# Kernel optimization log

Measured on AMD Instinct MI355X. Metric: run time of the kernel, lower is better.

## Reference

```python
import jax, jax.numpy as jnp
import numpy as np

T, B, D, O = 2048, 32, 512, 512


def setup_inputs() -> dict:
    key = jax.random.key(0)
    ks = jax.random.split(key, 12)
    s = 0.02
    return {
        "word": jax.random.normal(ks[0], (T, B, D), dtype=jnp.float32),
        "Wf": jax.random.normal(ks[1], (D, D), dtype=jnp.float32) * s,
        "bf": jax.random.normal(ks[2], (D,), dtype=jnp.float32) * s,
        "Wi": jax.random.normal(ks[3], (D, D), dtype=jnp.float32) * s,
        "bi": jax.random.normal(ks[4], (D,), dtype=jnp.float32) * s,
        "Wz": jax.random.normal(ks[5], (D, D), dtype=jnp.float32) * s,
        "bz": jax.random.normal(ks[6], (D,), dtype=jnp.float32) * s,
        "Wo": jax.random.normal(ks[7], (D, D), dtype=jnp.float32) * s,
        "bo": jax.random.normal(ks[8], (D,), dtype=jnp.float32) * s,
        "Wy": jax.random.normal(ks[9], (O, D), dtype=jnp.float32) * s,
        "by": jax.random.normal(ks[10], (O,), dtype=jnp.float32) * s,
    }


def reference(word, Wf, bf, Wi, bi, Wz, bz, Wo, bo, Wy, by):
    # Faithful to the original buggy module:
    #  - forward discards the updated cell state, so c == 0 every step and
    #    the zf gate (wf) never affects the output.
    #  - z and zo reuse wi(hidden) instead of wz/wo(hidden).
    #  - the same Linear is applied to letter and hidden, so bias is doubled
    #    in zi (and zf).
    Bsz, Dd = word.shape[1], word.shape[2]

    def step(h, x):  # h: [B, D], x: [B, D]
        hWi = h @ Wi.T                                  # reused by zi, z, zo
        zi = jax.nn.sigmoid(x @ Wi.T + hWi + 2.0 * bi)
        z = jax.nn.sigmoid(x @ Wz.T + bz + hWi + bi)
        zo = jax.nn.sigmoid(x @ Wo.T + bo + hWi + bi)
        c = zi * z                                      # zf * 0 + zi * z
        h_new = zo * jnp.tanh(c)
        return h_new, None

    h0 = jnp.zeros((Bsz, Dd), dtype=word.dtype)
    h_final, _ = jax.lax.scan(step, h0, word)
    # original computes wy(hidden) every step but only returns the last one
    output = h_final @ Wy.T + by                        # [B, O]
    return output
```

## Files before the change

kernel.cpp:

```cpp
#include <hip/hip_runtime.h>

typedef unsigned int u32;
typedef unsigned short u16;
typedef _Float16 f16;
typedef f16 f16x2 __attribute__((ext_vector_type(2)));

__device__ __forceinline__ float fdot2(u32 a, u32 b, float c) {
#if __has_builtin(__builtin_amdgcn_fdot2)
    return __builtin_amdgcn_fdot2(__builtin_bit_cast(f16x2, a),
                                  __builtin_bit_cast(f16x2, b), c, false);
#else
    f16x2 av = __builtin_bit_cast(f16x2, a), bv = __builtin_bit_cast(f16x2, b);
    c += (float)av[0] * (float)bv[0];
    c += (float)av[1] * (float)bv[1];
    return c;
#endif
}

__device__ __forceinline__ u32 pack2h(float a, float b) {
    f16x2 h; h[0] = (f16)a; h[1] = (f16)b;
    return __builtin_bit_cast(u32, h);
}
__device__ __forceinline__ float h2f(u16 x) { return (float)__builtin_bit_cast(f16, x); }
__device__ __forceinline__ u16 f2h(float x) { f16 h = (f16)x; return __builtin_bit_cast(u16, h); }

__device__ __forceinline__ float fexp(float x) {
#if __has_builtin(__builtin_amdgcn_exp2f)
    return __builtin_amdgcn_exp2f(x * 1.44269504088896f);
#else
    return __expf(x);
#endif
}
__device__ __forceinline__ float frcp(float x) {
#if __has_builtin(__builtin_amdgcn_rcpf)
    return __builtin_amdgcn_rcpf(x);
#else
    return 1.0f / x;
#endif
}
__device__ __forceinline__ float fsigmoid(float x) { return frcp(1.0f + fexp(-x)); }
__device__ __forceinline__ float ftanh_pos(float x) { return 1.0f - 2.0f * frcp(fexp(2.0f * x) + 1.0f); }

__global__ __launch_bounds__(512) void k0_pack(const float* __restrict__ Wi,
                                               const float* __restrict__ Wy,
                                               u32* __restrict__ Wpk,
                                               u32* __restrict__ Wypk) {
    const int p = blockIdx.x & 255;
    const int d = threadIdx.x;
    const float* src = (blockIdx.x < 256) ? Wi : Wy;
    u32* dst = (blockIdx.x < 256) ? Wpk : Wypk;
    float v0 = src[(size_t)d * 512 + 2 * p];
    float v1 = src[(size_t)d * 512 + 2 * p + 1];
    dst[(size_t)p * 512 + d] = pack2h(v0, v1);
}

__global__ __launch_bounds__(256) void k1_gates(
    const float* __restrict__ word,
    const float* __restrict__ Wi, const float* __restrict__ Wz, const float* __restrict__ Wo,
    const float* __restrict__ bi, const float* __restrict__ bz, const float* __restrict__ bo,
    u16* __restrict__ Xi, u16* __restrict__ Xz, u16* __restrict__ Xo)
{
    __shared__ u32 ws2[3][32][132];
    __shared__ u32 xs2[2][32][36];

    const int tid = threadIdx.x;
    const int d_l = tid & 63;
    const int bq  = tid >> 6;
    const int t0  = blockIdx.x * 2;
    const int d0  = blockIdx.y * 128;

    const float* Wg[3] = {Wi, Wz, Wo};

    float acc[2][2][8][3];
    #pragma unroll
    for (int tt = 0; tt < 2; ++tt)
        #pragma unroll
        for (int db = 0; db < 2; ++db)
            #pragma unroll
            for (int j = 0; j < 8; ++j)
                #pragma unroll
                for (int g = 0; g < 3; ++g) acc[tt][db][j][g] = 0.0f;

    for (int k0 = 0; k0 < 512; k0 += 64) {
        {
            const int p = tid & 31, bg = tid >> 5;
            #pragma unroll
            for (int tt = 0; tt < 2; ++tt)
                #pragma unroll
                for (int j = 0; j < 4; ++j) {
                    int b = bg * 4 + j;
                    const float2 v = *(const float2*)(word + (((size_t)(t0 + tt) * 32 + b) * 512 + k0 + 2 * p));
                    xs2[tt][p][b] = pack2h(v.x, v.y);
                }
        }
        {
            const int q = tid & 15, r = tid >> 4;
            #pragma unroll
            for (int g = 0; g < 3; ++g)
                #pragma unroll
                for (int s = 0; s < 8; ++s) {
                    int i = r + 16 * s;
                    const float4 v = *(const float4*)(Wg[g] + ((size_t)(d0 + i) * 512 + k0 + 4 * q));
                    ws2[g][2 * q + 0][i] = pack2h(v.x, v.y);
                    ws2[g][2 * q + 1][i] = pack2h(v.z, v.w);
                }
        }
        __syncthreads();
        #pragma unroll 2
        for (int p = 0; p < 32; ++p) {
            u32 x2[2][8];
            #pragma unroll
            for (int tt = 0; tt < 2; ++tt) {
                const uint4* xr = (const uint4*)&xs2[tt][p][bq * 8];
                uint4 xa = xr[0], xb = xr[1];
                x2[tt][0] = xa.x; x2[tt][1] = xa.y; x2[tt][2] = xa.z; x2[tt][3] = xa.w;
                x2[tt][4] = xb.x; x2[tt][5] = xb.y; x2[tt][6] = xb.z; x2[tt][7] = xb.w;
            }
            u32 w2[3][2];
            #pragma unroll
            for (int g = 0; g < 3; ++g) {
                w2[g][0] = ws2[g][p][d_l];
                w2[g][1] = ws2[g][p][d_l + 64];
            }
            #pragma unroll
            for (int tt = 0; tt < 2; ++tt)
                #pragma unroll
                for (int db = 0; db < 2; ++db)
                    #pragma unroll
                    for (int j = 0; j < 8; ++j)
                        #pragma unroll
                        for (int g = 0; g < 3; ++g)
                            acc[tt][db][j][g] = fdot2(x2[tt][j], w2[g][db], acc[tt][db][j][g]);
        }
        __syncthreads();
    }

    #pragma unroll
    for (int db = 0; db < 2; ++db) {
        const int d = d0 + 64 * db + d_l;
        const float b0 = 2.0f * bi[d];
        const float b1 = bz[d] + bi[d];
        const float b2 = bo[d] + bi[d];
        #pragma unroll
        for (int tt = 0; tt < 2; ++tt)
            #pragma unroll
            for (int j = 0; j < 8; ++j) {
                const size_t o = ((size_t)(t0 + tt) * 32 + (bq * 8 + j)) * 512 + d;
                Xi[o] = f2h(acc[tt][db][j][0] + b0);
                Xz[o] = f2h(acc[tt][db][j][1] + b1);
                Xo[o] = f2h(acc[tt][db][j][2] + b2);
            }
    }
}

__global__ __launch_bounds__(512, 2) void k2_recur(
    const u16* __restrict__ Xi, const u16* __restrict__ Xz, const u16* __restrict__ Xo,
    const u32* __restrict__ Wpk, const u32* __restrict__ Wypk,
    const float* __restrict__ by, float* __restrict__ out)
{
    __shared__ u32 wlds[28][512];
    __shared__ alignas(16) u16 hbuf[2][512];

    const int b = blockIdx.x;
    const int tid = threadIdx.x;

    u32 w[228];
    #pragma unroll
    for (int p = 0; p < 228; ++p) w[p] = Wpk[(size_t)p * 512 + tid];
    #pragma unroll
    for (int j = 0; j < 28; ++j) wlds[j][tid] = Wpk[(size_t)(228 + j) * 512 + tid];

    hbuf[0][tid] = (u16)0;
    __syncthreads();

    size_t idx0 = ((size_t)0 * 32 + b) * 512 + tid;
    u16 xi_c = Xi[idx0], xz_c = Xz[idx0], xo_c = Xo[idx0];

    for (int t = 0; t < 2048; ++t) {
        const int cur = t & 1, nxt = cur ^ 1;
        const int tn = (t + 1) & 2047;
        const size_t idxn = ((size_t)tn * 32 + b) * 512 + tid;
        u16 xi_n = Xi[idxn], xz_n = Xz[idxn], xo_n = Xo[idxn];

        const uint4* hv = (const uint4*)&hbuf[cur][0];
        float a0 = 0.f, a1 = 0.f, a2 = 0.f, a3 = 0.f;
        #pragma unroll
        for (int j = 0; j < 57; ++j) {
            uint4 hc = hv[j];
            a0 = fdot2(hc.x, w[4 * j + 0], a0);
            a1 = fdot2(hc.y, w[4 * j + 1], a1);
            a2 = fdot2(hc.z, w[4 * j + 2], a2);
            a3 = fdot2(hc.w, w[4 * j + 3], a3);
        }
        #pragma unroll
        for (int j = 57; j < 64; ++j) {
            uint4 hc = hv[j];
            const int q = 4 * (j - 57);
            a0 = fdot2(hc.x, wlds[q + 0][tid], a0);
            a1 = fdot2(hc.y, wlds[q + 1][tid], a1);
            a2 = fdot2(hc.z, wlds[q + 2][tid], a2);
            a3 = fdot2(hc.w, wlds[q + 3][tid], a3);
        }
        const float v = (a0 + a1) + (a2 + a3);

        const float zi = fsigmoid(h2f(xi_c) + v);
        const float z  = fsigmoid(h2f(xz_c) + v);
        const float zo = fsigmoid(h2f(xo_c) + v);
        const float hn = zo * ftanh_pos(zi * z);

        hbuf[nxt][tid] = f2h(hn);
        __syncthreads();

        xi_c = xi_n; xz_c = xz_n; xo_c = xo_n;
    }

    {
        const uint4* hv = (const uint4*)&hbuf[0][0];
        float a0 = 0.f, a1 = 0.f, a2 = 0.f, a3 = 0.f;
        #pragma unroll
        for (int j = 0; j < 64; ++j) {
            uint4 hc = hv[j];
            a0 = fdot2(hc.x, Wypk[(size_t)(4 * j + 0) * 512 + tid], a0);
            a1 = fdot2(hc.y, Wypk[(size_t)(4 * j + 1) * 512 + tid], a1);
            a2 = fdot2(hc.z, Wypk[(size_t)(4 * j + 2) * 512 + tid], a2);
            a3 = fdot2(hc.w, Wypk[(size_t)(4 * j + 3) * 512 + tid], a3);
        }
        out[(size_t)b * 512 + tid] = (a0 + a1) + (a2 + a3) + by[tid];
    }
}

extern "C" void kernel_launch(void* const* d_in, const int* in_sizes, int n_in,
                              void* d_out, int out_size, void* d_ws, size_t ws_size,
                              hipStream_t stream) {
    const float* word = (const float*)d_in[0];
    const float* Wi = (const float*)d_in[3];
    const float* bi = (const float*)d_in[4];
    const float* Wz = (const float*)d_in[5];
    const float* bz = (const float*)d_in[6];
    const float* Wo = (const float*)d_in[7];
    const float* bo = (const float*)d_in[8];
    const float* Wy = (const float*)d_in[9];
    const float* by = (const float*)d_in[10];
    float* out = (float*)d_out;

    char* ws = (char*)d_ws;
    const size_t XN = (size_t)2048 * 32 * 512 * sizeof(u16);
    u16* Xi = (u16*)(ws);
    u16* Xz = (u16*)(ws + XN);
    u16* Xo = (u16*)(ws + 2 * XN);
    u32* Wpk  = (u32*)(ws + 3 * XN);
    u32* Wypk = (u32*)(ws + 3 * XN + (size_t)524288);

    k0_pack<<<512, 512, 0, stream>>>(Wi, Wy, Wpk, Wypk);

    dim3 g1(1024, 4);
    k1_gates<<<g1, 256, 0, stream>>>(word, Wi, Wz, Wo, bi, bz, bo, Xi, Xz, Xo);

    k2_recur<<<32, 512, 0, stream>>>(Xi, Xz, Xo, Wpk, Wypk, by, out);
}
```

Before: 4.876 ms.

## Split recurrent matvec across 4-lane groups with DPP reduction; shrink gate K-tile

The recurrent kernel changes from one output per thread over the full K range to a layout where each group of 4 lanes covers 4 outputs. Each lane handles a quarter of K, and the partial sums are combined with DPP cross-lane adds. Each lane now reads only its K slice of h from LDS, which cuts per-step LDS broadcast reads of the hidden state roughly 4x. The cost is DPP shuffles and selects on the critical path, plus a new transposed weight packing. Separately, the gate GEMM K-tile drops from 64 to 32, halving its shared memory footprint to allow more occupancy.

After: 4.811 ms. About the same (-1.3%).

```diff
diff --git a/kernel.cpp b/kernel.cpp
--- a/kernel.cpp
+++ b/kernel.cpp
@@ -41,17 +41,29 @@
 __device__ __forceinline__ float fsigmoid(float x) { return frcp(1.0f + fexp(-x)); }
 __device__ __forceinline__ float ftanh_pos(float x) { return 1.0f - 2.0f * frcp(fexp(2.0f * x) + 1.0f); }
 
-__global__ __launch_bounds__(512) void k0_pack(const float* __restrict__ Wi,
+template <int CTRL>
+__device__ __forceinline__ float dpp_xor_add(float x) {
+    int y = __builtin_amdgcn_update_dpp(0, __builtin_bit_cast(int, x), CTRL, 0xF, 0xF, true);
+    return x + __builtin_bit_cast(float, y);
+}
+
+__global__ __launch_bounds__(256) void k0_pack(const float* __restrict__ Wi,
                                                const float* __restrict__ Wy,
-                                               u32* __restrict__ Wpk,
+                                               u32* __restrict__ WpkT,
                                                u32* __restrict__ Wypk) {
-    const int p = blockIdx.x & 255;
-    const int d = threadIdx.x;
-    const float* src = (blockIdx.x < 256) ? Wi : Wy;
-    u32* dst = (blockIdx.x < 256) ? Wpk : Wypk;
-    float v0 = src[(size_t)d * 512 + 2 * p];
-    float v1 = src[(size_t)d * 512 + 2 * p + 1];
-    dst[(size_t)p * 512 + d] = pack2h(v0, v1);
+    const int bx = blockIdx.x, tid = threadIdx.x;
+    if (bx < 512) {
+        const float2 v = *(const float2*)(Wi + (size_t)bx * 512 + 2 * tid);
+        WpkT[(size_t)bx * 256 + tid] = pack2h(v.x, v.y);
+    } else {
+        const int p = bx - 512;
+        #pragma unroll
+        for (int r = 0; r < 2; ++r) {
+            const int d = tid + 256 * r;
+            Wypk[(size_t)p * 512 + d] =
+                pack2h(Wy[(size_t)d * 512 + 2 * p], Wy[(size_t)d * 512 + 2 * p + 1]);
+        }
+    }
 }
 
 __global__ __launch_bounds__(256) void k1_gates(
@@ -60,8 +72,8 @@
     const float* __restrict__ bi, const float* __restrict__ bz, const float* __restrict__ bo,
     u16* __restrict__ Xi, u16* __restrict__ Xz, u16* __restrict__ Xo)
 {
-    __shared__ u32 ws2[3][32][132];
-    __shared__ u32 xs2[2][32][36];
+    __shared__ u32 ws2[3][16][132];
+    __shared__ u32 xs2[2][16][36];
 
     const int tid = threadIdx.x;
     const int d_l = tid & 63;
@@ -81,25 +93,25 @@
                 #pragma unroll
                 for (int g = 0; g < 3; ++g) acc[tt][db][j][g] = 0.0f;
 
-    for (int k0 = 0; k0 < 512; k0 += 64) {
+    for (int k0 = 0; k0 < 512; k0 += 32) {
         {
-            const int p = tid & 31, bg = tid >> 5;
+            const int p = tid & 15, bg = tid >> 4;
             #pragma unroll
             for (int tt = 0; tt < 2; ++tt)
                 #pragma unroll
-                for (int j = 0; j < 4; ++j) {
-                    int b = bg * 4 + j;
-                    const float2 v = *(const float2*)(word + (((size_t)(t0 + tt) * 32 + b) * 512 + k0 + 2 * p));
-                    xs2[tt][p][b] = pack2h(v.x, v.y);
+                for (int j = 0; j < 2; ++j) {
+                    const int bb = bg * 2 + j;
+                    const float2 v = *(const float2*)(word + (((size_t)(t0 + tt) * 32 + bb) * 512 + k0 + 2 * p));
+                    xs2[tt][p][bb] = pack2h(v.x, v.y);
                 }
         }
         {
-            const int q = tid & 15, r = tid >> 4;
+            const int q = tid & 7, r = tid >> 3;
             #pragma unroll
             for (int g = 0; g < 3; ++g)
                 #pragma unroll
-                for (int s = 0; s < 8; ++s) {
-                    int i = r + 16 * s;
+                for (int s = 0; s < 4; ++s) {
+                    const int i = r + 32 * s;
                     const float4 v = *(const float4*)(Wg[g] + ((size_t)(d0 + i) * 512 + k0 + 4 * q));
                     ws2[g][2 * q + 0][i] = pack2h(v.x, v.y);
                     ws2[g][2 * q + 1][i] = pack2h(v.z, v.w);
@@ -107,7 +119,7 @@
         }
         __syncthreads();
         #pragma unroll 2
-        for (int p = 0; p < 32; ++p) {
+        for (int p = 0; p < 16; ++p) {
             u32 x2[2][8];
             #pragma unroll
             for (int tt = 0; tt < 2; ++tt) {
@@ -155,25 +167,45 @@
 
 __global__ __launch_bounds__(512, 2) void k2_recur(
     const u16* __restrict__ Xi, const u16* __restrict__ Xz, const u16* __restrict__ Xo,
-    const u32* __restrict__ Wpk, const u32* __restrict__ Wypk,
+    const u32* __restrict__ WpkT, const u32* __restrict__ Wypk,
     const float* __restrict__ by, float* __restrict__ out)
 {
-    __shared__ u32 wlds[28][512];
+    __shared__ alignas(16) u32 wlds[7][2048];
     __shared__ alignas(16) u16 hbuf[2][512];
 
     const int b = blockIdx.x;
     const int tid = threadIdx.x;
-
-    u32 w[228];
+    const int kq = tid & 3, dg = tid >> 2;
+
+    u32 w[4][57];
     #pragma unroll
-    for (int p = 0; p < 228; ++p) w[p] = Wpk[(size_t)p * 512 + tid];
-    #pragma unroll
-    for (int j = 0; j < 28; ++j) wlds[j][tid] = Wpk[(size_t)(228 + j) * 512 + tid];
-
+    for (int j = 0; j < 4; ++j) {
+        const u32* row = WpkT + (size_t)(4 * dg + j) * 256 + 64 * kq;
+        const uint4* rv = (const uint4*)row;
+        #pragma unroll
+        for (int i = 0; i < 14; ++i) {
+            uint4 v = rv[i];
+            w[j][4 * i + 0] = v.x; w[j][4 * i + 1] = v.y;
+            w[j][4 * i + 2] = v.z; w[j][4 * i + 3] = v.w;
+        }
+        uint4 t14 = rv[14], t15 = rv[15];
+        w[j][56] = t14.x;
+        wlds[0][tid * 4 + j] = t14.y;
+        wlds[1][tid * 4 + j] = t14.z;
+        wlds[2][tid * 4 + j] = t14.w;
+        wlds[3][tid * 4 + j] = t15.x;
+        wlds[4][tid * 4 + j] = t15.y;
+        wlds[5][tid * 4 + j] = t15.z;
+        wlds[6][tid * 4 + j] = t15.w;
+    }
     hbuf[0][tid] = (u16)0;
     __syncthreads();
 
-    size_t idx0 = ((size_t)0 * 32 + b) * 512 + tid;
+    const uint4* hq0 = (const uint4*)&hbuf[0][0] + 16 * kq;
+    const uint4* hq1 = (const uint4*)&hbuf[1][0] + 16 * kq;
+    const uint4* wldv = (const uint4*)&wlds[0][0];
+
+    size_t idx0 = (size_t)b * 512 + tid;
     u16 xi_c = Xi[idx0], xz_c = Xz[idx0], xo_c = Xo[idx0];
 
     for (int t = 0; t < 2048; ++t) {
@@ -182,26 +214,64 @@
         const size_t idxn = ((size_t)tn * 32 + b) * 512 + tid;
         u16 xi_n = Xi[idxn], xz_n = Xz[idxn], xo_n = Xo[idxn];
 
-        const uint4* hv = (const uint4*)&hbuf[cur][0];
+        const uint4* hv = cur ? hq1 : hq0;
         float a0 = 0.f, a1 = 0.f, a2 = 0.f, a3 = 0.f;
         #pragma unroll
-        for (int j = 0; j < 57; ++j) {
-            uint4 hc = hv[j];
-            a0 = fdot2(hc.x, w[4 * j + 0], a0);
-            a1 = fdot2(hc.y, w[4 * j + 1], a1);
-            a2 = fdot2(hc.z, w[4 * j + 2], a2);
-            a3 = fdot2(hc.w, w[4 * j + 3], a3);
-        }
-        #pragma unroll
-        for (int j = 57; j < 64; ++j) {
-            uint4 hc = hv[j];
-            const int q = 4 * (j - 57);
-            a0 = fdot2(hc.x, wlds[q + 0][tid], a0);
-            a1 = fdot2(hc.y, wlds[q + 1][tid], a1);
-            a2 = fdot2(hc.z, wlds[q + 2][tid], a2);
-            a3 = fdot2(hc.w, wlds[q + 3][tid], a3);
-        }
-        const float v = (a0 + a1) + (a2 + a3);
+        for (int i = 0; i < 14; ++i) {
+            uint4 hc = hv[i];
+            a0 = fdot2(hc.x, w[0][4 * i + 0], a0);
+            a1 = fdot2(hc.x, w[1][4 * i + 0], a1);
+            a2 = fdot2(hc.x, w[2][4 * i + 0], a2);
+            a3 = fdot2(hc.x, w[3][4 * i + 0], a3);
+            a0 = fdot2(hc.y, w[0][4 * i + 1], a0);
+            a1 = fdot2(hc.y, w[1][4 * i + 1], a1);
+            a2 = fdot2(hc.y, w[2][4 * i + 1], a2);
+            a3 = fdot2(hc.y, w[3][4 * i + 1], a3);
+            a0 = fdot2(hc.z, w[0][4 * i + 2], a0);
+            a1 = fdot2(hc.z, w[1][4 * i + 2], a1);
+            a2 = fdot2(hc.z, w[2][4 * i + 2], a2);
+            a3 = fdot2(hc.z, w[3][4 * i + 2], a3);
+            a0 = fdot2(hc.w, w[0][4 * i + 3], a0);
+            a1 = fdot2(hc.w, w[1][4 * i + 3], a1);
+            a2 = fdot2(hc.w, w[2][4 * i + 3], a2);
+            a3 = fdot2(hc.w, w[3][4 * i + 3], a3);
+        }
+        {
+            uint4 h14 = hv[14], h15 = hv[15];
+            uint4 wl0 = wldv[0 * 512 + tid];
+            uint4 wl1 = wldv[1 * 512 + tid];
+            uint4 wl2 = wldv[2 * 512 + tid];
+            uint4 wl3 = wldv[3 * 512 + tid];
+            uint4 wl4 = wldv[4 * 512 + tid];
+            uint4 wl5 = wldv[5 * 512 + tid];
+            uint4 wl6 = wldv[6 * 512 + tid];
+            a0 = fdot2(h14.x, w[0][56], a0);
+            a1 = fdot2(h14.x, w[1][56], a1);
+            a2 = fdot2(h14.x, w[2][56], a2);
+            a3 = fdot2(h14.x, w[3][56], a3);
+            a0 = fdot2(h14.y, wl0.x, a0); a1 = fdot2(h14.y, wl0.y, a1);
+            a2 = fdot2(h14.y, wl0.z, a2); a3 = fdot2(h14.y, wl0.w, a3);
+            a0 = fdot2(h14.z, wl1.x, a0); a1 = fdot2(h14.z, wl1.y, a1);
+            a2 = fdot2(h14.z, wl1.z, a2); a3 = fdot2(h14.z, wl1.w, a3);
+            a0 = fdot2(h14.w, wl2.x, a0); a1 = fdot2(h14.w, wl2.y, a1);
+            a2 = fdot2(h14.w, wl2.z, a2); a3 = fdot2(h14.w, wl2.w, a3);
+            a0 = fdot2(h15.x, wl3.x, a0); a1 = fdot2(h15.x, wl3.y, a1);
+            a2 = fdot2(h15.x, wl3.z, a2); a3 = fdot2(h15.x, wl3.w, a3);
+            a0 = fdot2(h15.y, wl4.x, a0); a1 = fdot2(h15.y, wl4.y, a1);
+            a2 = fdot2(h15.y, wl4.z, a2); a3 = fdot2(h15.y, wl4.w, a3);
+            a0 = fdot2(h15.z, wl5.x, a0); a1 = fdot2(h15.z, wl5.y, a1);
+            a2 = fdot2(h15.z, wl5.z, a2); a3 = fdot2(h15.z, wl5.w, a3);
+            a0 = fdot2(h15.w, wl6.x, a0); a1 = fdot2(h15.w, wl6.y, a1);
+            a2 = fdot2(h15.w, wl6.z, a2); a3 = fdot2(h15.w, wl6.w, a3);
+        }
+        a0 = dpp_xor_add<0xB1>(a0); a1 = dpp_xor_add<0xB1>(a1);
+        a2 = dpp_xor_add<0xB1>(a2); a3 = dpp_xor_add<0xB1>(a3);
+        a0 = dpp_xor_add<0x4E>(a0); a1 = dpp_xor_add<0x4E>(a1);
+        a2 = dpp_xor_add<0x4E>(a2); a3 = dpp_xor_add<0x4E>(a3);
+        float v = a0;
+        v = (kq == 1) ? a1 : v;
+        v = (kq == 2) ? a2 : v;
+        v = (kq == 3) ? a3 : v;
 
         const float zi = fsigmoid(h2f(xi_c) + v);
         const float z  = fsigmoid(h2f(xz_c) + v);
@@ -218,12 +288,12 @@
         const uint4* hv = (const uint4*)&hbuf[0][0];
         float a0 = 0.f, a1 = 0.f, a2 = 0.f, a3 = 0.f;
         #pragma unroll
-        for (int j = 0; j < 64; ++j) {
-            uint4 hc = hv[j];
-            a0 = fdot2(hc.x, Wypk[(size_t)(4 * j + 0) * 512 + tid], a0);
-            a1 = fdot2(hc.y, Wypk[(size_t)(4 * j + 1) * 512 + tid], a1);
-            a2 = fdot2(hc.z, Wypk[(size_t)(4 * j + 2) * 512 + tid], a2);
-            a3 = fdot2(hc.w, Wypk[(size_t)(4 * j + 3) * 512 + tid], a3);
+        for (int i = 0; i < 64; ++i) {
+            uint4 hc = hv[i];
+            a0 = fdot2(hc.x, Wypk[(size_t)(4 * i + 0) * 512 + tid], a0);
+            a1 = fdot2(hc.y, Wypk[(size_t)(4 * i + 1) * 512 + tid], a1);
+            a2 = fdot2(hc.z, Wypk[(size_t)(4 * i + 2) * 512 + tid], a2);
+            a3 = fdot2(hc.w, Wypk[(size_t)(4 * i + 3) * 512 + tid], a3);
         }
         out[(size_t)b * 512 + tid] = (a0 + a1) + (a2 + a3) + by[tid];
     }
@@ -248,13 +318,13 @@
     u16* Xi = (u16*)(ws);
     u16* Xz = (u16*)(ws + XN);
     u16* Xo = (u16*)(ws + 2 * XN);
-    u32* Wpk  = (u32*)(ws + 3 * XN);
+    u32* WpkT = (u32*)(ws + 3 * XN);
     u32* Wypk = (u32*)(ws + 3 * XN + (size_t)524288);
 
-    k0_pack<<<512, 512, 0, stream>>>(Wi, Wy, Wpk, Wypk);
+    k0_pack<<<768, 256, 0, stream>>>(Wi, Wy, WpkT, Wypk);
 
     dim3 g1(1024, 4);
     k1_gates<<<g1, 256, 0, stream>>>(word, Wi, Wz, Wo, bi, bz, bo, Xi, Xz, Xo);
 
-    k2_recur<<<32, 512, 0, stream>>>(Xi, Xz, Xo, Wpk, Wypk, by, out);
-}
+    k2_recur<<<32, 512, 0, stream>>>(Xi, Xz, Xo, WpkT, Wypk, by, out);
+}
```

## Split recurrence across two blocks per batch with global partial-sum exchange

Applied to the files above, without the earlier changes.

The recurrent matvec for each batch row is now split over two workgroups. Each one keeps half of a transposed, packed Wi in registers as uint4, computes a partial dot product, and swaps it with its partner every step through tagged 64-bit atomic stores and spin-loads in global memory. This halves the per-step dot-product work and the register pressure, and drops the LDS spill of weights, at the cost of an inter-workgroup round trip per timestep that may cross XCDs. The input-gate GEMM also moves to 32-wide K chunks with a swizzled uint4 LDS weight layout, and the pack kernel gains a coalesced transposed layout for Wi.

Result: faster. 4.449 ms (-8.7%).

```diff
diff --git a/kernel.cpp b/kernel.cpp
--- a/kernel.cpp
+++ b/kernel.cpp
@@ -2,6 +2,7 @@
 
 typedef unsigned int u32;
 typedef unsigned short u16;
+typedef unsigned long long u64;
 typedef _Float16 f16;
 typedef f16 f16x2 __attribute__((ext_vector_type(2)));
 
@@ -41,17 +42,23 @@
 __device__ __forceinline__ float fsigmoid(float x) { return frcp(1.0f + fexp(-x)); }
 __device__ __forceinline__ float ftanh_pos(float x) { return 1.0f - 2.0f * frcp(fexp(2.0f * x) + 1.0f); }
 
-__global__ __launch_bounds__(512) void k0_pack(const float* __restrict__ Wi,
+__global__ __launch_bounds__(256) void k0_pack(const float* __restrict__ Wi,
                                                const float* __restrict__ Wy,
-                                               u32* __restrict__ Wpk,
+                                               u32* __restrict__ WpkT,
                                                u32* __restrict__ Wypk) {
-    const int p = blockIdx.x & 255;
-    const int d = threadIdx.x;
-    const float* src = (blockIdx.x < 256) ? Wi : Wy;
-    u32* dst = (blockIdx.x < 256) ? Wpk : Wypk;
-    float v0 = src[(size_t)d * 512 + 2 * p];
-    float v1 = src[(size_t)d * 512 + 2 * p + 1];
-    dst[(size_t)p * 512 + d] = pack2h(v0, v1);
+    const int bx = blockIdx.x, tid = threadIdx.x;
+    if (bx < 512) {
+        const float2 v = *(const float2*)(Wi + (size_t)bx * 512 + 2 * tid);
+        WpkT[(size_t)bx * 256 + tid] = pack2h(v.x, v.y);
+    } else {
+        const int p = bx - 512;
+        #pragma unroll
+        for (int r = 0; r < 2; ++r) {
+            const int d = tid + 256 * r;
+            Wypk[(size_t)p * 512 + d] =
+                pack2h(Wy[(size_t)d * 512 + 2 * p], Wy[(size_t)d * 512 + 2 * p + 1]);
+        }
+    }
 }
 
 __global__ __launch_bounds__(256) void k1_gates(
@@ -60,8 +67,8 @@
     const float* __restrict__ bi, const float* __restrict__ bz, const float* __restrict__ bo,
     u16* __restrict__ Xi, u16* __restrict__ Xz, u16* __restrict__ Xo)
 {
-    __shared__ u32 ws2[3][32][132];
-    __shared__ u32 xs2[2][32][36];
+    __shared__ uint4 ws2v[3][128][4];
+    __shared__ u32 xs2[2][16][36];
 
     const int tid = threadIdx.x;
     const int d_l = tid & 63;
@@ -81,56 +88,72 @@
                 #pragma unroll
                 for (int g = 0; g < 3; ++g) acc[tt][db][j][g] = 0.0f;
 
-    for (int k0 = 0; k0 < 512; k0 += 64) {
+    for (int k0c = 0; k0c < 512; k0c += 32) {
         {
-            const int p = tid & 31, bg = tid >> 5;
+            const int p = tid & 15, bg = tid >> 4;
             #pragma unroll
             for (int tt = 0; tt < 2; ++tt)
                 #pragma unroll
-                for (int j = 0; j < 4; ++j) {
-                    int b = bg * 4 + j;
-                    const float2 v = *(const float2*)(word + (((size_t)(t0 + tt) * 32 + b) * 512 + k0 + 2 * p));
-                    xs2[tt][p][b] = pack2h(v.x, v.y);
+                for (int j = 0; j < 2; ++j) {
+                    const int bb = bg * 2 + j;
+                    const float2 v = *(const float2*)(word + (((size_t)(t0 + tt) * 32 + bb) * 512 + k0c + 2 * p));
+                    xs2[tt][p][bb] = pack2h(v.x, v.y);
                 }
         }
         {
-            const int q = tid & 15, r = tid >> 4;
+            #pragma unroll
+            for (int cc = 0; cc < 6; ++cc) {
+                const int c = tid + 256 * cc;
+                const int g = c >> 9, r = c & 511, pg = r >> 7, i = r & 127;
+                const float* src = Wg[g] + (size_t)(d0 + i) * 512 + k0c + 8 * pg;
+                const float4 v0 = ((const float4*)src)[0];
+                const float4 v1 = ((const float4*)src)[1];
+                uint4 cell;
+                cell.x = pack2h(v0.x, v0.y); cell.y = pack2h(v0.z, v0.w);
+                cell.z = pack2h(v1.x, v1.y); cell.w = pack2h(v1.z, v1.w);
+                ws2v[g][i][(pg + (i >> 2)) & 3] = cell;
+            }
+        }
+        __syncthreads();
+        #pragma unroll
+        for (int pg = 0; pg < 4; ++pg) {
+            uint4 wc[3][2];
             #pragma unroll
             for (int g = 0; g < 3; ++g)
                 #pragma unroll
-                for (int s = 0; s < 8; ++s) {
-                    int i = r + 16 * s;
-                    const float4 v = *(const float4*)(Wg[g] + ((size_t)(d0 + i) * 512 + k0 + 4 * q));
-                    ws2[g][2 * q + 0][i] = pack2h(v.x, v.y);
-                    ws2[g][2 * q + 1][i] = pack2h(v.z, v.w);
+                for (int db = 0; db < 2; ++db) {
+                    const int d = d_l + 64 * db;
+                    wc[g][db] = ws2v[g][d][(pg + (d >> 2)) & 3];
                 }
-        }
-        __syncthreads();
-        #pragma unroll 2
-        for (int p = 0; p < 32; ++p) {
-            u32 x2[2][8];
-            #pragma unroll
-            for (int tt = 0; tt < 2; ++tt) {
-                const uint4* xr = (const uint4*)&xs2[tt][p][bq * 8];
-                uint4 xa = xr[0], xb = xr[1];
-                x2[tt][0] = xa.x; x2[tt][1] = xa.y; x2[tt][2] = xa.z; x2[tt][3] = xa.w;
-                x2[tt][4] = xb.x; x2[tt][5] = xb.y; x2[tt][6] = xb.z; x2[tt][7] = xb.w;
+            #pragma unroll
+            for (int p = 0; p < 4; ++p) {
+                const int pair = 4 * pg + p;
+                u32 x2[2][8];
+                #pragma unroll
+                for (int tt = 0; tt < 2; ++tt) {
+                    const uint4* xr = (const uint4*)&xs2[tt][pair][bq * 8];
+                    uint4 xa = xr[0], xb = xr[1];
+                    x2[tt][0] = xa.x; x2[tt][1] = xa.y; x2[tt][2] = xa.z; x2[tt][3] = xa.w;
+                    x2[tt][4] = xb.x; x2[tt][5] = xb.y; x2[tt][6] = xb.z; x2[tt][7] = xb.w;
+                }
+                u32 w[3][2];
+                #pragma unroll
+                for (int g = 0; g < 3; ++g)
+                    #pragma unroll
+                    for (int db = 0; db < 2; ++db) {
+                        const uint4 v = wc[g][db];
+                        w[g][db] = (p == 0) ? v.x : (p == 1) ? v.y : (p == 2) ? v.z : v.w;
+                    }
+                #pragma unroll
+                for (int tt = 0; tt < 2; ++tt)
+                    #pragma unroll
+                    for (int db = 0; db < 2; ++db)
+                        #pragma unroll
+                        for (int j = 0; j < 8; ++j)
+                            #pragma unroll
+                            for (int g = 0; g < 3; ++g)
+                                acc[tt][db][j][g] = fdot2(x2[tt][j], w[g][db], acc[tt][db][j][g]);
             }
-            u32 w2[3][2];
-            #pragma unroll
-            for (int g = 0; g < 3; ++g) {
-                w2[g][0] = ws2[g][p][d_l];
-                w2[g][1] = ws2[g][p][d_l + 64];
-            }
-            #pragma unroll
-            for (int tt = 0; tt < 2; ++tt)
-                #pragma unroll
-                for (int db = 0; db < 2; ++db)
-                    #pragma unroll
-                    for (int j = 0; j < 8; ++j)
-                        #pragma unroll
-                        for (int g = 0; g < 3; ++g)
-                            acc[tt][db][j][g] = fdot2(x2[tt][j], w2[g][db], acc[tt][db][j][g]);
         }
         __syncthreads();
     }
@@ -153,79 +176,92 @@
     }
 }
 
-__global__ __launch_bounds__(512, 2) void k2_recur(
+__global__ __launch_bounds__(512, 1) void k2_recur(
     const u16* __restrict__ Xi, const u16* __restrict__ Xz, const u16* __restrict__ Xo,
-    const u32* __restrict__ Wpk, const u32* __restrict__ Wypk,
+    const u32* __restrict__ WpkT, const u32* __restrict__ Wypk,
+    u64* __restrict__ exch,
     const float* __restrict__ by, float* __restrict__ out)
 {
-    __shared__ u32 wlds[28][512];
-    __shared__ alignas(16) u16 hbuf[2][512];
-
-    const int b = blockIdx.x;
-    const int tid = threadIdx.x;
-
-    u32 w[228];
+    __shared__ alignas(16) u16 hb[2][256];
+    __shared__ alignas(16) u16 hfull[512];
+
+    const int bid  = blockIdx.x;
+    const int b    = bid >> 1;
+    const int half = bid & 1;
+    const int tid  = threadIdx.x;
+
+    const uint4* WpkT4 = (const uint4*)WpkT;
+    uint4 w[32];
     #pragma unroll
-    for (int p = 0; p < 228; ++p) w[p] = Wpk[(size_t)p * 512 + tid];
-    #pragma unroll
-    for (int j = 0; j < 28; ++j) wlds[j][tid] = Wpk[(size_t)(228 + j) * 512 + tid];
-
-    hbuf[0][tid] = (u16)0;
+    for (int i = 0; i < 32; ++i) w[i] = WpkT4[(size_t)tid * 64 + half * 32 + i];
+
+    if (tid < 256) hb[0][tid] = (u16)0;
     __syncthreads();
 
-    size_t idx0 = ((size_t)0 * 32 + b) * 512 + tid;
-    u16 xi_c = Xi[idx0], xz_c = Xz[idx0], xo_c = Xo[idx0];
-
+    u64* eo = exch + ((size_t)(b * 2 + half) * 2) * 512 + tid;
+    const u64* ei = exch + ((size_t)(b * 2 + (half ^ 1)) * 2) * 512 + tid;
+
+    const int ownhalf = ((tid >> 8) == half);
+    const int hloc = tid & 255;
+
+    u16 xi_c = Xi[(size_t)b * 512 + tid];
+    u16 xz_c = Xz[(size_t)b * 512 + tid];
+    u16 xo_c = Xo[(size_t)b * 512 + tid];
+
+    float hn = 0.0f;
     for (int t = 0; t < 2048; ++t) {
-        const int cur = t & 1, nxt = cur ^ 1;
+        const int par = t & 1;
         const int tn = (t + 1) & 2047;
-        const size_t idxn = ((size_t)tn * 32 + b) * 512 + tid;
-        u16 xi_n = Xi[idxn], xz_n = Xz[idxn], xo_n = Xo[idxn];
-
-        const uint4* hv = (const uint4*)&hbuf[cur][0];
+        const size_t xb = ((size_t)tn * 32 + b) * 512 + tid;
+        const u16 xi_n = Xi[xb], xz_n = Xz[xb], xo_n = Xo[xb];
+
+        const uint4* hv = (const uint4*)&hb[par][0];
         float a0 = 0.f, a1 = 0.f, a2 = 0.f, a3 = 0.f;
         #pragma unroll
-        for (int j = 0; j < 57; ++j) {
-            uint4 hc = hv[j];
-            a0 = fdot2(hc.x, w[4 * j + 0], a0);
-            a1 = fdot2(hc.y, w[4 * j + 1], a1);
-            a2 = fdot2(hc.z, w[4 * j + 2], a2);
-            a3 = fdot2(hc.w, w[4 * j + 3], a3);
-        }
-        #pragma unroll
-        for (int j = 57; j < 64; ++j) {
-            uint4 hc = hv[j];
-            const int q = 4 * (j - 57);
-            a0 = fdot2(hc.x, wlds[q + 0][tid], a0);
-            a1 = fdot2(hc.y, wlds[q + 1][tid], a1);
-            a2 = fdot2(hc.z, wlds[q + 2][tid], a2);
-            a3 = fdot2(hc.w, wlds[q + 3][tid], a3);
-        }
-        const float v = (a0 + a1) + (a2 + a3);
+        for (int i = 0; i < 32; ++i) {
+            const uint4 hc = hv[i];
+            a0 = fdot2(hc.x, w[i].x, a0);
+            a1 = fdot2(hc.y, w[i].y, a1);
+            a2 = fdot2(hc.z, w[i].z, a2);
+            a3 = fdot2(hc.w, w[i].w, a3);
+        }
+        const float p = (a0 + a1) + (a2 + a3);
+
+        const u64 msg = ((u64)(u32)(t + 1) << 32) | (u64)__builtin_bit_cast(u32, p);
+        __hip_atomic_store(eo + (size_t)par * 512, msg,
+                           __ATOMIC_RELAXED, __HIP_MEMORY_SCOPE_AGENT);
+        u64 m;
+        do {
+            m = __hip_atomic_load(ei + (size_t)par * 512,
+                                  __ATOMIC_RELAXED, __HIP_MEMORY_SCOPE_AGENT);
+        } while ((u32)(m >> 32) != (u32)(t + 1));
+        const float v = p + __builtin_bit_cast(float, (u32)m);
 
         const float zi = fsigmoid(h2f(xi_c) + v);
         const float z  = fsigmoid(h2f(xz_c) + v);
         const float zo = fsigmoid(h2f(xo_c) + v);
-        const float hn = zo * ftanh_pos(zi * z);
-
-        hbuf[nxt][tid] = f2h(hn);
+        hn = zo * ftanh_pos(zi * z);
+
+        if (ownhalf) hb[par ^ 1][hloc] = f2h(hn);
         __syncthreads();
 
         xi_c = xi_n; xz_c = xz_n; xo_c = xo_n;
     }
 
+    hfull[tid] = f2h(hn);
+    __syncthreads();
     {
-        const uint4* hv = (const uint4*)&hbuf[0][0];
-        float a0 = 0.f, a1 = 0.f, a2 = 0.f, a3 = 0.f;
-        #pragma unroll
-        for (int j = 0; j < 64; ++j) {
-            uint4 hc = hv[j];
-            a0 = fdot2(hc.x, Wypk[(size_t)(4 * j + 0) * 512 + tid], a0);
-            a1 = fdot2(hc.y, Wypk[(size_t)(4 * j + 1) * 512 + tid], a1);
-            a2 = fdot2(hc.z, Wypk[(size_t)(4 * j + 2) * 512 + tid], a2);
-            a3 = fdot2(hc.w, Wypk[(size_t)(4 * j + 3) * 512 + tid], a3);
-        }
-        out[(size_t)b * 512 + tid] = (a0 + a1) + (a2 + a3) + by[tid];
+        const uint4* hv = (const uint4*)&hfull[0];
+        float e0 = 0.f, e1 = 0.f, e2 = 0.f, e3 = 0.f;
+        #pragma unroll 8
+        for (int i = 0; i < 64; ++i) {
+            const uint4 hc = hv[i];
+            e0 = fdot2(hc.x, Wypk[(size_t)(4 * i + 0) * 512 + tid], e0);
+            e1 = fdot2(hc.y, Wypk[(size_t)(4 * i + 1) * 512 + tid], e1);
+            e2 = fdot2(hc.z, Wypk[(size_t)(4 * i + 2) * 512 + tid], e2);
+            e3 = fdot2(hc.w, Wypk[(size_t)(4 * i + 3) * 512 + tid], e3);
+        }
+        out[(size_t)b * 512 + tid] = (e0 + e1) + (e2 + e3) + by[tid];
     }
 }
 
@@ -248,13 +284,14 @@
     u16* Xi = (u16*)(ws);
     u16* Xz = (u16*)(ws + XN);
     u16* Xo = (u16*)(ws + 2 * XN);
-    u32* Wpk  = (u32*)(ws + 3 * XN);
+    u32* WpkT = (u32*)(ws + 3 * XN);
     u32* Wypk = (u32*)(ws + 3 * XN + (size_t)524288);
-
-    k0_pack<<<512, 512, 0, stream>>>(Wi, Wy, Wpk, Wypk);
+    u64* exch = (u64*)(ws + 3 * XN + (size_t)2 * 524288);
+
+    k0_pack<<<768, 256, 0, stream>>>(Wi, Wy, WpkT, Wypk);
 
     dim3 g1(1024, 4);
     k1_gates<<<g1, 256, 0, stream>>>(word, Wi, Wz, Wo, bi, bz, bo, Xi, Xz, Xo);
 
-    k2_recur<<<32, 512, 0, stream>>>(Xi, Xz, Xo, Wpk, Wypk, by, out);
-}
+    k2_recur<<<64, 512, 0, stream>>>(Xi, Xz, Xo, WpkT, Wypk, exch, by, out);
+}
```
